# Optimization experiments

Measured on AMD Instinct MI355X. Metric: run time of the kernel, lower is better.

Reference implementation:

```python
import jax, jax.numpy as jnp
import numpy as np

NUM_LEVELS = 4
RADIUS = 4


def avg_pool2(x):
    # x: [N, H, W] -> [N, H//2, W//2] (kernel 2, stride 2 average pool)
    n, h, w = x.shape
    return x.reshape(n, h // 2, 2, w // 2, 2).mean(axis=(2, 4))


def bilinear_sample(img, x, y):
    # img: [N, H, W]; x, y: [N, S, S] absolute pixel coords (align_corners=True),
    # zero padding outside [0, W-1] x [0, H-1] (matches F.grid_sample defaults).
    n, h, w = img.shape
    x0 = jnp.floor(x)
    y0 = jnp.floor(y)
    wx1 = x - x0
    wy1 = y - y0
    wx0 = 1.0 - wx1
    wy0 = 1.0 - wy1
    nidx = jnp.arange(n)[:, None, None]

    def gather(yi, xi):
        valid = (xi >= 0) & (xi <= w - 1) & (yi >= 0) & (yi <= h - 1)
        xic = jnp.clip(xi, 0, w - 1).astype(jnp.int32)
        yic = jnp.clip(yi, 0, h - 1).astype(jnp.int32)
        return jnp.where(valid, img[nidx, yic, xic], 0.0)

    return (gather(y0, x0) * wy0 * wx0 + gather(y0, x0 + 1) * wy0 * wx1
            + gather(y0 + 1, x0) * wy1 * wx0 + gather(y0 + 1, x0 + 1) * wy1 * wx1)


def setup_inputs() -> dict:
    key = jax.random.key(0)
    k1, k2, k3 = jax.random.split(key, 3)
    b, c, h, w = 2, 256, 64, 64
    fmap1 = jax.random.normal(k1, (b, c, h, w), dtype=jnp.float32)
    fmap2 = jax.random.normal(k2, (b, c, h, w), dtype=jnp.float32)
    # absolute pixel (x, y) coordinates in [0, W-1] / [0, H-1]
    centroids_coords = jax.random.uniform(k3, (b, 2, h, w), dtype=jnp.float32) * (w - 1)
    return {"fmap1": fmap1, "fmap2": fmap2, "centroids_coords": centroids_coords}


def reference(fmap1, fmap2, centroids_coords):
    b, c, h1, w1 = fmap1.shape
    h2, w2 = fmap2.shape[-2:]
    # correlation volume: [b, h1*w1, h2*w2] / sqrt(c)
    f1 = fmap1.reshape(b, c, h1 * w1)
    f2 = fmap2.reshape(b, c, h2 * w2)
    corr = jnp.einsum('bcm,bcn->bmn', f1, f2) / jnp.sqrt(jnp.asarray(c, fmap1.dtype))
    corr = corr.reshape(b * h1 * w1, h2, w2)

    pyramid = [corr]
    for _ in range(NUM_LEVELS - 1):
        corr = avg_pool2(corr)
        pyramid.append(corr)

    side = 2 * RADIUS + 1
    di = jnp.linspace(-RADIUS, RADIUS, side)
    # delta[..., 0] = di (added to x), delta[..., 1] = dj (added to y) -- as in source
    delta = jnp.stack(jnp.meshgrid(di, di, indexing='ij'), axis=-1)  # [S, S, 2]

    cc = centroids_coords.transpose(0, 2, 3, 1).reshape(b * h1 * w1, 1, 1, 2)
    feats = []
    for lvl, vol in enumerate(pyramid):
        grid = cc / (2.0 ** lvl) + delta[None]  # [N, S, S, 2]
        sampled = bilinear_sample(vol, grid[..., 0], grid[..., 1])  # [N, S, S]
        feats.append(sampled.reshape(b, h1, w1, side * side))
    # [b, num_levels*side^2, h1, w1]
    return jnp.concatenate(feats, axis=-1).transpose(0, 3, 1, 2)
```

## Files before the change

### kernel.cpp

```cpp
#include <hip/hip_runtime.h>
#include <stdint.h>

#define M_DIM 4096
#define K_DIM 256

typedef __attribute__((ext_vector_type(8))) short bf16x8;
typedef __attribute__((ext_vector_type(4))) float f32x4;

static __device__ __forceinline__ float bf2f(unsigned short u){
  unsigned int x = ((unsigned int)u) << 16; float f;
  __builtin_memcpy(&f, &x, 4); return f;
}
static __device__ __forceinline__ unsigned short f2bf(float f){
  unsigned int x; __builtin_memcpy(&x, &f, 4);
  unsigned int r = x + 0x7fffu + ((x >> 16) & 1u);
  return (unsigned short)(r >> 16);
}
static __device__ __forceinline__ void gld16(const void* g, void* l){
  __builtin_amdgcn_global_load_lds(
      (const __attribute__((address_space(1))) unsigned int*)g,
      (__attribute__((address_space(3))) unsigned int*)l, 16, 0, 0);
}

__global__ void k_transpose_cast(const float* __restrict__ in,
                                 unsigned short* __restrict__ out, float scale){
  __shared__ float lds[64][65];
  int b = blockIdx.z, c0 = blockIdx.y * 64, m0 = blockIdx.x * 64;
  const float* ib = in + (size_t)b * K_DIM * M_DIM;
  unsigned short* ob = out + (size_t)b * M_DIM * K_DIM;
  int t = threadIdx.x, r = t >> 6, j = t & 63;
#pragma unroll
  for (int k = 0; k < 16; k++)
    lds[r + k*4][j] = ib[(size_t)(c0 + r + k*4) * M_DIM + m0 + j];
  __syncthreads();
#pragma unroll
  for (int k = 0; k < 16; k++)
    ob[(size_t)(m0 + r + k*4) * K_DIM + c0 + j] = f2bf(lds[j][r + k*4] * scale);
}

__global__ void k_pool(const unsigned short* __restrict__ src,
                       unsigned short* __restrict__ dst, int wd){
  int t = threadIdx.x;
  int idx = blockIdx.x * 4 + (t >> 6);
  int l = t & 63;
  int per = wd * wd;
  int b = idx / per, rem = idx - b * per;
  int y = rem / wd, x = rem - y * wd;
  int ws2 = wd * 2;
  const unsigned short* sb = src + (size_t)b * per * 4 * K_DIM;
  unsigned short* db = dst + (size_t)b * per * K_DIM;
  int c = l * 4;
  size_t r00 = ((size_t)(2*y) * ws2 + 2*x) * K_DIM + c;
  size_t r01 = r00 + K_DIM;
  size_t r10 = r00 + (size_t)ws2 * K_DIM;
  size_t r11 = r10 + K_DIM;
  uint2 va = *(const uint2*)(sb + r00);
  uint2 vb = *(const uint2*)(sb + r01);
  uint2 vc = *(const uint2*)(sb + r10);
  uint2 vd = *(const uint2*)(sb + r11);
  float s0 = (bf2f(va.x & 0xffff) + bf2f(vb.x & 0xffff) + bf2f(vc.x & 0xffff) + bf2f(vd.x & 0xffff)) * 0.25f;
  float s1 = (bf2f(va.x >> 16)  + bf2f(vb.x >> 16)  + bf2f(vc.x >> 16)  + bf2f(vd.x >> 16))  * 0.25f;
  float s2 = (bf2f(va.y & 0xffff) + bf2f(vb.y & 0xffff) + bf2f(vc.y & 0xffff) + bf2f(vd.y & 0xffff)) * 0.25f;
  float s3 = (bf2f(va.y >> 16)  + bf2f(vb.y >> 16)  + bf2f(vc.y >> 16)  + bf2f(vd.y >> 16))  * 0.25f;
  uint2 o;
  o.x = (unsigned)f2bf(s0) | ((unsigned)f2bf(s1) << 16);
  o.y = (unsigned)f2bf(s2) | ((unsigned)f2bf(s3) << 16);
  *(uint2*)(db + (size_t)rem * K_DIM + c) = o;
}

__global__ void k_gemm(const unsigned short* __restrict__ A,
                       const unsigned short* __restrict__ B,
                       unsigned short* __restrict__ C, int N){
  __shared__ __align__(16) unsigned short As[128 * 32];
  __shared__ __align__(16) unsigned short Bs[128 * 32];
  int b = blockIdx.z;
  const unsigned short* Ab = A + (size_t)b * M_DIM * K_DIM;
  const unsigned short* Bb = B + (size_t)b * N * K_DIM;
  unsigned short* Cb = C + (size_t)b * M_DIM * N;
  int m0 = blockIdx.y * 128, n0 = blockIdx.x * 128;
  int t = threadIdx.x;
  int wave = t >> 6, lane = t & 63;
  int wm = (wave >> 1) * 64, wn = (wave & 1) * 64;
  int srow = t >> 2, scol = (t & 3) * 8;
  int fr = lane & 15, fk = (lane >> 4) * 8;
  f32x4 acc[4][4];
#pragma unroll
  for (int i = 0; i < 4; i++)
#pragma unroll
    for (int j = 0; j < 4; j++) acc[i][j] = (f32x4){0.f, 0.f, 0.f, 0.f};

  int nr0 = n0 + srow;      if (nr0 > N - 1) nr0 = N - 1;
  int nr1 = n0 + srow + 64; if (nr1 > N - 1) nr1 = N - 1;
  const unsigned short* ga0 = Ab + (size_t)(m0 + srow) * K_DIM + scol;
  const unsigned short* ga1 = Ab + (size_t)(m0 + srow + 64) * K_DIM + scol;
  const unsigned short* gb0 = Bb + (size_t)nr0 * K_DIM + scol;
  const unsigned short* gb1 = Bb + (size_t)nr1 * K_DIM + scol;

  for (int kt = 0; kt < K_DIM; kt += 32){
    __syncthreads();
    gld16(ga0 + kt, (unsigned short*)As + t * 8);
    gld16(ga1 + kt, (unsigned short*)As + t * 8 + 2048);
    gld16(gb0 + kt, (unsigned short*)Bs + t * 8);
    gld16(gb1 + kt, (unsigned short*)Bs + t * 8 + 2048);
    asm volatile("s_waitcnt vmcnt(0)" ::: "memory");
    __syncthreads();
    bf16x8 af[4], bfv[4];
#pragma unroll
    for (int i = 0; i < 4; i++)
      af[i] = *(const bf16x8*)((unsigned short*)As + (wm + i*16 + fr) * 32 + fk);
#pragma unroll
    for (int j = 0; j < 4; j++)
      bfv[j] = *(const bf16x8*)((unsigned short*)Bs + (wn + j*16 + fr) * 32 + fk);
#pragma unroll
    for (int i = 0; i < 4; i++)
#pragma unroll
      for (int j = 0; j < 4; j++)
        acc[i][j] = __builtin_amdgcn_mfma_f32_16x16x32_bf16(af[i], bfv[j], acc[i][j], 0, 0, 0);
  }

  int cr = (lane >> 4) * 4, ccol = lane & 15;
#pragma unroll
  for (int i = 0; i < 4; i++){
#pragma unroll
    for (int j = 0; j < 4; j++){
      int col = n0 + wn + j*16 + ccol;
      if (col < N){
        size_t base = (size_t)(m0 + wm + i*16 + cr) * N + col;
#pragma unroll
        for (int r = 0; r < 4; r++)
          Cb[base + (size_t)r * N] = f2bf(acc[i][j][r]);
      }
    }
  }
}

__global__ void k_sample(const unsigned short* __restrict__ p0,
                         const unsigned short* __restrict__ p1,
                         const unsigned short* __restrict__ p2,
                         const unsigned short* __restrict__ p3,
                         const float* __restrict__ cc, float* __restrict__ out){
  int i = blockIdx.x, b = blockIdx.y, lvl = blockIdx.z;
  int j = threadIdx.x;
  const unsigned short* corr; int wl;
  if (lvl == 0)      { corr = p0; wl = 64; }
  else if (lvl == 1) { corr = p1; wl = 32; }
  else if (lvl == 2) { corr = p2; wl = 16; }
  else               { corr = p3; wl = 8;  }
  float inv = 1.0f / (float)(1 << lvl);
  int m = i * 64 + j;
  const unsigned short* rowp = corr + (size_t)(b * M_DIM + m) * (wl * wl);
  float cx = cc[((size_t)(b*2 + 0) * 64 + i) * 64 + j];
  float cy = cc[((size_t)(b*2 + 1) * 64 + i) * 64 + j];
  float x = cx * inv, y = cy * inv;
  float x0f = floorf(x), y0f = floorf(y);
  int x0 = (int)x0f, y0 = (int)y0f;
  float fx = x - x0f, fy = y - y0f;
  float C[10][10];
#pragma unroll
  for (int v = 0; v < 10; v++){
    int ry = y0 - 4 + v;
    bool vy = (unsigned)ry < (unsigned)wl;
    int ryc = ry < 0 ? 0 : (ry > wl - 1 ? wl - 1 : ry);
#pragma unroll
    for (int u = 0; u < 10; u++){
      int rx = x0 - 4 + u;
      bool vx = (unsigned)rx < (unsigned)wl;
      int rxc = rx < 0 ? 0 : (rx > wl - 1 ? wl - 1 : rx);
      float val = bf2f(rowp[ryc * wl + rxc]);
      C[v][u] = (vx && vy) ? val : 0.0f;
    }
  }
  float wx1 = fx, wx0 = 1.0f - fx, wy1 = fy, wy0 = 1.0f - fy;
  size_t obase = (size_t)b * 324 + lvl * 81;
#pragma unroll
  for (int a = 0; a < 9; a++){
#pragma unroll
    for (int d = 0; d < 9; d++){
      float val = wy0 * (wx0 * C[d][a]   + wx1 * C[d][a+1])
                + wy1 * (wx0 * C[d+1][a] + wx1 * C[d+1][a+1]);
      out[((obase + a*9 + d) * 64 + i) * 64 + j] = val;
    }
  }
}

extern "C" void kernel_launch(void* const* d_in, const int* in_sizes, int n_in,
                              void* d_out, int out_size, void* d_ws, size_t ws_size,
                              hipStream_t stream){
  (void)in_sizes; (void)n_in; (void)out_size; (void)ws_size;
  const float* f1 = (const float*)d_in[0];
  const float* f2 = (const float*)d_in[1];
  const float* cc = (const float*)d_in[2];
  float* out = (float*)d_out;
  char* ws = (char*)d_ws;
  unsigned short* A  = (unsigned short*)(ws + 0);
  unsigned short* B0 = (unsigned short*)(ws + 4194304);
  unsigned short* B1 = (unsigned short*)(ws + 8388608);
  unsigned short* B2 = (unsigned short*)(ws + 9437184);
  unsigned short* B3 = (unsigned short*)(ws + 9699328);
  unsigned short* C0 = (unsigned short*)(ws + 9764864);
  unsigned short* C1 = (unsigned short*)(ws + 76873728);
  unsigned short* C2 = (unsigned short*)(ws + 93650944);
  unsigned short* C3 = (unsigned short*)(ws + 97845248);

  dim3 bt(256);
  k_transpose_cast<<<dim3(64, 4, 2), bt, 0, stream>>>(f1, A, 0.0625f);
  k_transpose_cast<<<dim3(64, 4, 2), bt, 0, stream>>>(f2, B0, 1.0f);
  k_pool<<<dim3(512), bt, 0, stream>>>(B0, B1, 32);
  k_pool<<<dim3(128), bt, 0, stream>>>(B1, B2, 16);
  k_pool<<<dim3(32),  bt, 0, stream>>>(B2, B3, 8);
  k_gemm<<<dim3(32, 32, 2), bt, 0, stream>>>(A, B0, C0, 4096);
  k_gemm<<<dim3(8, 32, 2),  bt, 0, stream>>>(A, B1, C1, 1024);
  k_gemm<<<dim3(2, 32, 2),  bt, 0, stream>>>(A, B2, C2, 256);
  k_gemm<<<dim3(1, 32, 2),  bt, 0, stream>>>(A, B3, C3, 64);
  k_sample<<<dim3(64, 2, 4), dim3(64), 0, stream>>>(C0, C1, C2, C3, cc, out);
}
```

Baseline: 141.2 us.

## Merge launches, double-buffer GEMM LDS, and split sampling across eight waves

Merges the two transpose-casts into one launch, the three pool launches into one (each level pooled directly from level 0), and the four GEMMs into one launch with a level-dispatching grid. The GEMM LDS tiles become double-buffered so the next k-slice's global-to-LDS load overlaps the current MFMAs. The sampling kernel now uses 512 threads per block, with each wave handling one or two output rows, and loads the correlation window as paired 32-bit reads. Together these cut launch overhead, raise sampling parallelism and hide GEMM load latency, at the cost of more pooling reads for coarse levels and more LDS per GEMM block.

```diff
diff --git a/kernel.cpp b/kernel.cpp
--- a/kernel.cpp
+++ b/kernel.cpp
@@ -4,17 +4,18 @@
 #define M_DIM 4096
 #define K_DIM 256
 
+typedef unsigned short us;
 typedef __attribute__((ext_vector_type(8))) short bf16x8;
 typedef __attribute__((ext_vector_type(4))) float f32x4;
 
-static __device__ __forceinline__ float bf2f(unsigned short u){
-  unsigned int x = ((unsigned int)u) << 16; float f;
+static __device__ __forceinline__ float bf2f(unsigned int u){
+  unsigned int x = u << 16; float f;
   __builtin_memcpy(&f, &x, 4); return f;
 }
-static __device__ __forceinline__ unsigned short f2bf(float f){
+static __device__ __forceinline__ us f2bf(float f){
   unsigned int x; __builtin_memcpy(&x, &f, 4);
   unsigned int r = x + 0x7fffu + ((x >> 16) & 1u);
-  return (unsigned short)(r >> 16);
+  return (us)(r >> 16);
 }
 static __device__ __forceinline__ void gld16(const void* g, void* l){
   __builtin_amdgcn_global_load_lds(
@@ -22,12 +23,18 @@
       (__attribute__((address_space(3))) unsigned int*)l, 16, 0, 0);
 }
 
-__global__ void k_transpose_cast(const float* __restrict__ in,
-                                 unsigned short* __restrict__ out, float scale){
+__global__ void k_transpose_cast(const float* __restrict__ f1,
+                                 const float* __restrict__ f2,
+                                 us* __restrict__ A, us* __restrict__ B0){
   __shared__ float lds[64][65];
-  int b = blockIdx.z, c0 = blockIdx.y * 64, m0 = blockIdx.x * 64;
+  int z = blockIdx.z;
+  int b = z & 1, which = z >> 1;
+  const float* in = which ? f2 : f1;
+  us* out = which ? B0 : A;
+  float scale = which ? 1.0f : 0.0625f;
+  int c0 = blockIdx.y * 64, m0 = blockIdx.x * 64;
   const float* ib = in + (size_t)b * K_DIM * M_DIM;
-  unsigned short* ob = out + (size_t)b * M_DIM * K_DIM;
+  us* ob = out + (size_t)b * M_DIM * K_DIM;
   int t = threadIdx.x, r = t >> 6, j = t & 63;
 #pragma unroll
   for (int k = 0; k < 16; k++)
@@ -38,46 +45,55 @@
     ob[(size_t)(m0 + r + k*4) * K_DIM + c0 + j] = f2bf(lds[j][r + k*4] * scale);
 }
 
-__global__ void k_pool(const unsigned short* __restrict__ src,
-                       unsigned short* __restrict__ dst, int wd){
+__global__ void k_pool_all(const us* __restrict__ B0, us* __restrict__ B1,
+                           us* __restrict__ B2, us* __restrict__ B3){
+  int bid = blockIdx.x;
+  us* dst; int wd, f;
+  if (bid < 512)      { dst = B1; wd = 32; f = 2; }
+  else if (bid < 640) { bid -= 512; dst = B2; wd = 16; f = 4; }
+  else                { bid -= 640; dst = B3; wd = 8;  f = 8; }
   int t = threadIdx.x;
-  int idx = blockIdx.x * 4 + (t >> 6);
+  int idx = bid * 4 + (t >> 6);
   int l = t & 63;
   int per = wd * wd;
   int b = idx / per, rem = idx - b * per;
   int y = rem / wd, x = rem - y * wd;
-  int ws2 = wd * 2;
-  const unsigned short* sb = src + (size_t)b * per * 4 * K_DIM;
-  unsigned short* db = dst + (size_t)b * per * K_DIM;
-  int c = l * 4;
-  size_t r00 = ((size_t)(2*y) * ws2 + 2*x) * K_DIM + c;
-  size_t r01 = r00 + K_DIM;
-  size_t r10 = r00 + (size_t)ws2 * K_DIM;
-  size_t r11 = r10 + K_DIM;
-  uint2 va = *(const uint2*)(sb + r00);
-  uint2 vb = *(const uint2*)(sb + r01);
-  uint2 vc = *(const uint2*)(sb + r10);
-  uint2 vd = *(const uint2*)(sb + r11);
-  float s0 = (bf2f(va.x & 0xffff) + bf2f(vb.x & 0xffff) + bf2f(vc.x & 0xffff) + bf2f(vd.x & 0xffff)) * 0.25f;
-  float s1 = (bf2f(va.x >> 16)  + bf2f(vb.x >> 16)  + bf2f(vc.x >> 16)  + bf2f(vd.x >> 16))  * 0.25f;
-  float s2 = (bf2f(va.y & 0xffff) + bf2f(vb.y & 0xffff) + bf2f(vc.y & 0xffff) + bf2f(vd.y & 0xffff)) * 0.25f;
-  float s3 = (bf2f(va.y >> 16)  + bf2f(vb.y >> 16)  + bf2f(vc.y >> 16)  + bf2f(vd.y >> 16))  * 0.25f;
+  const us* sb = B0 + (size_t)b * 4096 * K_DIM;
+  float s0 = 0, s1 = 0, s2 = 0, s3 = 0;
+  for (int dy = 0; dy < f; dy++)
+    for (int dx = 0; dx < f; dx++){
+      size_t off = ((size_t)(f*y + dy) * 64 + (f*x + dx)) * K_DIM + l * 4;
+      uint2 v = *(const uint2*)(sb + off);
+      s0 += bf2f(v.x & 0xffff); s1 += bf2f(v.x >> 16);
+      s2 += bf2f(v.y & 0xffff); s3 += bf2f(v.y >> 16);
+    }
+  float inv = 1.0f / (float)(f * f);
   uint2 o;
-  o.x = (unsigned)f2bf(s0) | ((unsigned)f2bf(s1) << 16);
-  o.y = (unsigned)f2bf(s2) | ((unsigned)f2bf(s3) << 16);
-  *(uint2*)(db + (size_t)rem * K_DIM + c) = o;
-}
-
-__global__ void k_gemm(const unsigned short* __restrict__ A,
-                       const unsigned short* __restrict__ B,
-                       unsigned short* __restrict__ C, int N){
-  __shared__ __align__(16) unsigned short As[128 * 32];
-  __shared__ __align__(16) unsigned short Bs[128 * 32];
+  o.x = (unsigned)f2bf(s0*inv) | ((unsigned)f2bf(s1*inv) << 16);
+  o.y = (unsigned)f2bf(s2*inv) | ((unsigned)f2bf(s3*inv) << 16);
+  us* db = dst + (size_t)b * per * K_DIM;
+  *(uint2*)(db + (size_t)rem * K_DIM + l * 4) = o;
+}
+
+__global__ __launch_bounds__(256) void k_gemm_all(
+    const us* __restrict__ A,
+    const us* __restrict__ B0, const us* __restrict__ B1,
+    const us* __restrict__ B2, const us* __restrict__ B3,
+    us* __restrict__ C0, us* __restrict__ C1,
+    us* __restrict__ C2, us* __restrict__ C3){
+  __shared__ __align__(16) us As[2][4096];
+  __shared__ __align__(16) us Bs[2][4096];
+  int bx = blockIdx.x;
+  const us* B; us* C; int N, n0;
+  if (bx < 32)      { B = B0; C = C0; N = 4096; n0 = bx * 128; }
+  else if (bx < 40) { B = B1; C = C1; N = 1024; n0 = (bx - 32) * 128; }
+  else if (bx < 42) { B = B2; C = C2; N = 256;  n0 = (bx - 40) * 128; }
+  else              { B = B3; C = C3; N = 64;   n0 = 0; }
   int b = blockIdx.z;
-  const unsigned short* Ab = A + (size_t)b * M_DIM * K_DIM;
-  const unsigned short* Bb = B + (size_t)b * N * K_DIM;
-  unsigned short* Cb = C + (size_t)b * M_DIM * N;
-  int m0 = blockIdx.y * 128, n0 = blockIdx.x * 128;
+  const us* Ab = A + (size_t)b * M_DIM * K_DIM;
+  const us* Bb = B + (size_t)b * N * K_DIM;
+  us* Cb = C + (size_t)b * M_DIM * N;
+  int m0 = blockIdx.y * 128;
   int t = threadIdx.x;
   int wave = t >> 6, lane = t & 63;
   int wm = (wave >> 1) * 64, wn = (wave & 1) * 64;
@@ -91,31 +107,42 @@
 
   int nr0 = n0 + srow;      if (nr0 > N - 1) nr0 = N - 1;
   int nr1 = n0 + srow + 64; if (nr1 > N - 1) nr1 = N - 1;
-  const unsigned short* ga0 = Ab + (size_t)(m0 + srow) * K_DIM + scol;
-  const unsigned short* ga1 = Ab + (size_t)(m0 + srow + 64) * K_DIM + scol;
-  const unsigned short* gb0 = Bb + (size_t)nr0 * K_DIM + scol;
-  const unsigned short* gb1 = Bb + (size_t)nr1 * K_DIM + scol;
-
-  for (int kt = 0; kt < K_DIM; kt += 32){
-    __syncthreads();
-    gld16(ga0 + kt, (unsigned short*)As + t * 8);
-    gld16(ga1 + kt, (unsigned short*)As + t * 8 + 2048);
-    gld16(gb0 + kt, (unsigned short*)Bs + t * 8);
-    gld16(gb1 + kt, (unsigned short*)Bs + t * 8 + 2048);
+  const us* ga0 = Ab + (size_t)(m0 + srow) * K_DIM + scol;
+  const us* ga1 = Ab + (size_t)(m0 + srow + 64) * K_DIM + scol;
+  const us* gb0 = Bb + (size_t)nr0 * K_DIM + scol;
+  const us* gb1 = Bb + (size_t)nr1 * K_DIM + scol;
+
+  gld16(ga0, &As[0][t*8]);
+  gld16(ga1, &As[0][t*8 + 2048]);
+  gld16(gb0, &Bs[0][t*8]);
+  gld16(gb1, &Bs[0][t*8 + 2048]);
+  asm volatile("s_waitcnt vmcnt(0)" ::: "memory");
+  __syncthreads();
+
+  int cur = 0;
+  for (int it = 0; it < 8; ++it){
+    if (it < 7){
+      int kt = (it + 1) * 32;
+      gld16(ga0 + kt, &As[cur^1][t*8]);
+      gld16(ga1 + kt, &As[cur^1][t*8 + 2048]);
+      gld16(gb0 + kt, &Bs[cur^1][t*8]);
+      gld16(gb1 + kt, &Bs[cur^1][t*8 + 2048]);
+    }
+    bf16x8 af[4], bfv[4];
+#pragma unroll
+    for (int i = 0; i < 4; i++)
+      af[i] = *(const bf16x8*)&As[cur][(wm + i*16 + fr) * 32 + fk];
+#pragma unroll
+    for (int j = 0; j < 4; j++)
+      bfv[j] = *(const bf16x8*)&Bs[cur][(wn + j*16 + fr) * 32 + fk];
+#pragma unroll
+    for (int i = 0; i < 4; i++)
+#pragma unroll
+      for (int j = 0; j < 4; j++)
+        acc[i][j] = __builtin_amdgcn_mfma_f32_16x16x32_bf16(af[i], bfv[j], acc[i][j], 0, 0, 0);
     asm volatile("s_waitcnt vmcnt(0)" ::: "memory");
     __syncthreads();
-    bf16x8 af[4], bfv[4];
-#pragma unroll
-    for (int i = 0; i < 4; i++)
-      af[i] = *(const bf16x8*)((unsigned short*)As + (wm + i*16 + fr) * 32 + fk);
-#pragma unroll
-    for (int j = 0; j < 4; j++)
-      bfv[j] = *(const bf16x8*)((unsigned short*)Bs + (wn + j*16 + fr) * 32 + fk);
-#pragma unroll
-    for (int i = 0; i < 4; i++)
-#pragma unroll
-      for (int j = 0; j < 4; j++)
-        acc[i][j] = __builtin_amdgcn_mfma_f32_16x16x32_bf16(af[i], bfv[j], acc[i][j], 0, 0, 0);
+    cur ^= 1;
   }
 
   int cr = (lane >> 4) * 4, ccol = lane & 15;
@@ -134,51 +161,74 @@
   }
 }
 
-__global__ void k_sample(const unsigned short* __restrict__ p0,
-                         const unsigned short* __restrict__ p1,
-                         const unsigned short* __restrict__ p2,
-                         const unsigned short* __restrict__ p3,
-                         const float* __restrict__ cc, float* __restrict__ out){
+__global__ __launch_bounds__(512) void k_sample(
+    const us* __restrict__ p0, const us* __restrict__ p1,
+    const us* __restrict__ p2, const us* __restrict__ p3,
+    const float* __restrict__ cc, float* __restrict__ out){
   int i = blockIdx.x, b = blockIdx.y, lvl = blockIdx.z;
-  int j = threadIdx.x;
-  const unsigned short* corr; int wl;
+  int t = threadIdx.x;
+  int w = t >> 6, j = t & 63;
+  const us* corr; int wl;
   if (lvl == 0)      { corr = p0; wl = 64; }
   else if (lvl == 1) { corr = p1; wl = 32; }
   else if (lvl == 2) { corr = p2; wl = 16; }
   else               { corr = p3; wl = 8;  }
   float inv = 1.0f / (float)(1 << lvl);
   int m = i * 64 + j;
-  const unsigned short* rowp = corr + (size_t)(b * M_DIM + m) * (wl * wl);
+  const us* rowp = corr + (size_t)(b * M_DIM + m) * (wl * wl);
   float cx = cc[((size_t)(b*2 + 0) * 64 + i) * 64 + j];
   float cy = cc[((size_t)(b*2 + 1) * 64 + i) * 64 + j];
   float x = cx * inv, y = cy * inv;
   float x0f = floorf(x), y0f = floorf(y);
   int x0 = (int)x0f, y0 = (int)y0f;
   float fx = x - x0f, fy = y - y0f;
-  float C[10][10];
-#pragma unroll
-  for (int v = 0; v < 10; v++){
-    int ry = y0 - 4 + v;
-    bool vy = (unsigned)ry < (unsigned)wl;
+
+  int d_lo  = (w == 0) ? 0 : w + 1;
+  int d_cnt = (w == 0) ? 2 : 1;
+  int nrows = d_cnt + 1;
+
+  int bxi = x0 - 4;
+  int a0 = bxi & ~1;
+  int par = bxi & 1;
+
+  float Cw[3][12];
+#pragma unroll
+  for (int v = 0; v < 3; v++){
+    int ry = y0 - 4 + d_lo + v;
+    bool vy = ((unsigned)ry < (unsigned)wl) && (v < nrows);
     int ryc = ry < 0 ? 0 : (ry > wl - 1 ? wl - 1 : ry);
+    const us* rp = rowp + ryc * wl;
+#pragma unroll
+    for (int k = 0; k < 6; k++){
+      int e = a0 + 2*k;
+      int ec = e < 0 ? 0 : (e > wl - 2 ? wl - 2 : e);
+      unsigned dv = *(const unsigned*)(rp + ec);
+      Cw[v][2*k]   = vy ? bf2f(dv & 0xffff) : 0.0f;
+      Cw[v][2*k+1] = vy ? bf2f(dv >> 16)    : 0.0f;
+    }
+  }
+  float T[3][10];
+#pragma unroll
+  for (int v = 0; v < 3; v++)
 #pragma unroll
     for (int u = 0; u < 10; u++){
-      int rx = x0 - 4 + u;
-      bool vx = (unsigned)rx < (unsigned)wl;
-      int rxc = rx < 0 ? 0 : (rx > wl - 1 ? wl - 1 : rx);
-      float val = bf2f(rowp[ryc * wl + rxc]);
-      C[v][u] = (vx && vy) ? val : 0.0f;
-    }
-  }
+      float val = par ? Cw[v][u+1] : Cw[v][u];
+      bool vx = (unsigned)(bxi + u) < (unsigned)wl;
+      T[v][u] = vx ? val : 0.0f;
+    }
+
   float wx1 = fx, wx0 = 1.0f - fx, wy1 = fy, wy0 = 1.0f - fy;
-  size_t obase = (size_t)b * 324 + lvl * 81;
-#pragma unroll
-  for (int a = 0; a < 9; a++){
-#pragma unroll
-    for (int d = 0; d < 9; d++){
-      float val = wy0 * (wx0 * C[d][a]   + wx1 * C[d][a+1])
-                + wy1 * (wx0 * C[d+1][a] + wx1 * C[d+1][a+1]);
-      out[((obase + a*9 + d) * 64 + i) * 64 + j] = val;
+  size_t ob = (size_t)b * 324 + lvl * 81;
+#pragma unroll
+  for (int dd = 0; dd < 2; dd++){
+    if (dd < d_cnt){
+      int d = d_lo + dd;
+#pragma unroll
+      for (int a = 0; a < 9; a++){
+        float val = wy0 * (wx0 * T[dd][a]   + wx1 * T[dd][a+1])
+                  + wy1 * (wx0 * T[dd+1][a] + wx1 * T[dd+1][a+1]);
+        out[((ob + a*9 + d) * 64 + i) * 64 + j] = val;
+      }
     }
   }
 }
@@ -192,25 +242,18 @@
   const float* cc = (const float*)d_in[2];
   float* out = (float*)d_out;
   char* ws = (char*)d_ws;
-  unsigned short* A  = (unsigned short*)(ws + 0);
-  unsigned short* B0 = (unsigned short*)(ws + 4194304);
-  unsigned short* B1 = (unsigned short*)(ws + 8388608);
-  unsigned short* B2 = (unsigned short*)(ws + 9437184);
-  unsigned short* B3 = (unsigned short*)(ws + 9699328);
-  unsigned short* C0 = (unsigned short*)(ws + 9764864);
-  unsigned short* C1 = (unsigned short*)(ws + 76873728);
-  unsigned short* C2 = (unsigned short*)(ws + 93650944);
-  unsigned short* C3 = (unsigned short*)(ws + 97845248);
-
-  dim3 bt(256);
-  k_transpose_cast<<<dim3(64, 4, 2), bt, 0, stream>>>(f1, A, 0.0625f);
-  k_transpose_cast<<<dim3(64, 4, 2), bt, 0, stream>>>(f2, B0, 1.0f);
-  k_pool<<<dim3(512), bt, 0, stream>>>(B0, B1, 32);
-  k_pool<<<dim3(128), bt, 0, stream>>>(B1, B2, 16);
-  k_pool<<<dim3(32),  bt, 0, stream>>>(B2, B3, 8);
-  k_gemm<<<dim3(32, 32, 2), bt, 0, stream>>>(A, B0, C0, 4096);
-  k_gemm<<<dim3(8, 32, 2),  bt, 0, stream>>>(A, B1, C1, 1024);
-  k_gemm<<<dim3(2, 32, 2),  bt, 0, stream>>>(A, B2, C2, 256);
-  k_gemm<<<dim3(1, 32, 2),  bt, 0, stream>>>(A, B3, C3, 64);
-  k_sample<<<dim3(64, 2, 4), dim3(64), 0, stream>>>(C0, C1, C2, C3, cc, out);
-}
+  us* A  = (us*)(ws + 0);
+  us* B0 = (us*)(ws + 4194304);
+  us* B1 = (us*)(ws + 8388608);
+  us* B2 = (us*)(ws + 9437184);
+  us* B3 = (us*)(ws + 9699328);
+  us* C0 = (us*)(ws + 9764864);
+  us* C1 = (us*)(ws + 76873728);
+  us* C2 = (us*)(ws + 93650944);
+  us* C3 = (us*)(ws + 97845248);
+
+  k_transpose_cast<<<dim3(64, 4, 4), dim3(256), 0, stream>>>(f1, f2, A, B0);
+  k_pool_all<<<dim3(672), dim3(256), 0, stream>>>(B0, B1, B2, B3);
+  k_gemm_all<<<dim3(43, 32, 2), dim3(256), 0, stream>>>(A, B0, B1, B2, B3, C0, C1, C2, C3);
+  k_sample<<<dim3(64, 2, 4), dim3(512), 0, stream>>>(C0, C1, C2, C3, cc, out);
+}
```

New measurement: 160.7 us. +13.8%, slower.
